# Optimization experiments

Hardware: AMD Instinct MI355X
Metric: run time of the kernel (lower is better)

Reference implementation:

```python
import jax, jax.numpy as jnp
import numpy as np

B, S, D = 4, 2048, 1024
H, HD = 16, 64  # heads, head_dim; H*HD == D


def setup_inputs() -> dict:
    key = jax.random.key(0)
    k_x, k_qkv, k_proj = jax.random.split(key, 3)
    x = jax.random.normal(k_x, (B, S, D), dtype=jnp.float32)
    # init scale ~ 1/sqrt(fan_in) to keep activations sane
    w_qkv = jax.random.normal(k_qkv, (D, 3 * H * HD), dtype=jnp.float32) / np.sqrt(D)
    b_qkv = jnp.zeros((3 * H * HD,), dtype=jnp.float32)
    w_proj = jax.random.normal(k_proj, (H * HD, D), dtype=jnp.float32) / np.sqrt(H * HD)
    b_proj = jnp.zeros((D,), dtype=jnp.float32)
    return {"x": x, "w_qkv": w_qkv, "b_qkv": b_qkv, "w_proj": w_proj,
            "b_proj": b_proj, "layer_idx": 0}


def reference(x, w_qkv, b_qkv, w_proj, b_proj, layer_idx):
    # c_attn: [B,S,D] -> [B,S,3*H*HD]
    qkv = x @ w_qkv + b_qkv
    qkv = qkv.reshape(B, S, 3, H, HD)
    q, k, v = qkv[:, :, 0], qkv[:, :, 1], qkv[:, :, 2]  # each [B,S,H,HD]

    scale = jax.lax.rsqrt(float(HD))  # scale_by_inverse_layer_idx=False
    # scores: [B,H,S_q,S_k]
    scores = jnp.einsum("bqhd,bkhd->bhqk", q, k) * scale
    causal = jnp.tril(jnp.ones((S, S), dtype=jnp.bool_))
    scores = jnp.where(causal, scores, -1e9)
    attn = jax.nn.softmax(scores, axis=-1)  # dropout is identity (inference)

    out = jnp.einsum("bhqk,bkhd->bqhd", attn, v).reshape(B, S, H * HD)
    return out @ w_proj + b_proj
```

## Files before the change

### kernel.cpp

```cpp
#include <hip/hip_runtime.h>

typedef __attribute__((ext_vector_type(8))) short short8;
typedef __attribute__((ext_vector_type(4))) float f32x4;
typedef __attribute__((ext_vector_type(16))) float f32x16;
typedef __attribute__((ext_vector_type(4))) float flt4;
typedef __attribute__((ext_vector_type(4))) unsigned int u32x4;
typedef unsigned short bfbits;

#define DEVI __device__ __forceinline__

constexpr int Bc = 4, Sc = 2048, Dc = 1024, Hc = 16, HDc = 64;
constexpr int M1 = Bc * Sc;
constexpr int N1 = 3 * Hc * HDc;
constexpr int Kd = Dc;

typedef __attribute__((address_space(1))) const unsigned int gas_u32;
typedef __attribute__((address_space(3))) unsigned int las_u32;

DEVI void gld_lds16(const void* g, void* l) {
  __builtin_amdgcn_global_load_lds((gas_u32*)g, (las_u32*)l, 16, 0, 0);
}

DEVI unsigned short f2bf(float f) {
  unsigned int x = __builtin_bit_cast(unsigned int, f);
  x = x + 0x7fffu + ((x >> 16) & 1u);
  return (unsigned short)(x >> 16);
}

DEVI f32x4 zero4() { f32x4 z = {0.f, 0.f, 0.f, 0.f}; return z; }

DEVI short8 lds8(const void* base, int byteoff) {
  return *(const short8*)((const char*)base + byteoff);
}

DEVI unsigned int cvtpk_bf16(float lo, float hi) {
  unsigned int r;
  asm("v_cvt_pk_bf16_f32 %0, %1, %2" : "=v"(r) : "v"(lo), "v"(hi));
  return r;
}

DEVI void pl32swap(unsigned int& dst, unsigned int& src) {
  asm volatile("v_permlane32_swap_b32 %0, %1" : "+v"(dst), "+v"(src));
}

__global__ void cast_x_kernel(const float* __restrict__ in, bfbits* __restrict__ out, int n8) {
  int i = blockIdx.x * 256 + threadIdx.x;
  if (i >= n8) return;
  const flt4* p = (const flt4*)in;
  flt4 a = p[(size_t)2 * i];
  flt4 b = p[(size_t)2 * i + 1];
  short8 r;
  r[0] = (short)f2bf(a[0]); r[1] = (short)f2bf(a[1]);
  r[2] = (short)f2bf(a[2]); r[3] = (short)f2bf(a[3]);
  r[4] = (short)f2bf(b[0]); r[5] = (short)f2bf(b[1]);
  r[6] = (short)f2bf(b[2]); r[7] = (short)f2bf(b[3]);
  *(short8*)(out + (size_t)8 * i) = r;
}

__global__ void transpose_cast_kernel(const float* __restrict__ in, bfbits* __restrict__ out,
                                      int R, int C) {
  __shared__ float tile[32][33];
  int bc = blockIdx.x * 32, br = blockIdx.y * 32;
  int tx = threadIdx.x & 31, ty = threadIdx.x >> 5;
#pragma unroll
  for (int i = 0; i < 32; i += 8)
    tile[ty + i][tx] = in[(size_t)(br + ty + i) * C + bc + tx];
  __syncthreads();
#pragma unroll
  for (int i = 0; i < 32; i += 8)
    out[(size_t)(bc + ty + i) * R + br + tx] = f2bf(tile[tx][ty + i]);
}

template <int EPI>
__global__ __launch_bounds__(256, 2) void gemm_bt_kernel(
    const bfbits* __restrict__ A, const bfbits* __restrict__ Bt,
    const float* __restrict__ bias,
    bfbits* __restrict__ outQ, bfbits* __restrict__ outK, bfbits* __restrict__ outV,
    float* __restrict__ outF, int M, int N, int K) {
  __shared__ bfbits sA[128 * 64];
  __shared__ bfbits sB[128 * 64];
  const int t = threadIdx.x;
  const int wid = t >> 6, l = t & 63;
  const int lr = l & 15, lg = l >> 4;
  const int m0 = blockIdx.y * 128, n0 = blockIdx.x * 128;
  const int wr = (wid >> 1) * 64, wc = (wid & 1) * 64;

  f32x4 acc[4][4];
#pragma unroll
  for (int i = 0; i < 4; ++i)
#pragma unroll
    for (int j = 0; j < 4; ++j) acc[i][j] = zero4();

  const int row_s = t >> 3;
  const int grp_s = t & 7;

  for (int kt = 0; kt < K; kt += 64) {
#pragma unroll
    for (int i = 0; i < 4; ++i) {
      int row = i * 32 + row_s;
      int grp = grp_s ^ (row & 7);
      gld_lds16(A + (size_t)(m0 + row) * K + kt + grp * 8, sA + i * 2048 + wid * 512);
      gld_lds16(Bt + (size_t)(n0 + row) * K + kt + grp * 8, sB + i * 2048 + wid * 512);
    }
    __syncthreads();
#pragma unroll
    for (int ks = 0; ks < 2; ++ks) {
      short8 af[4], bf[4];
#pragma unroll
      for (int i = 0; i < 4; ++i) {
        int rA = wr + i * 16 + lr;
        af[i] = lds8(sA, rA * 128 + (((ks * 4 + lg) ^ (rA & 7)) << 4));
        int rB = wc + i * 16 + lr;
        bf[i] = lds8(sB, rB * 128 + (((ks * 4 + lg) ^ (rB & 7)) << 4));
      }
#pragma unroll
      for (int i = 0; i < 4; ++i)
#pragma unroll
        for (int j = 0; j < 4; ++j)
          acc[i][j] = __builtin_amdgcn_mfma_f32_16x16x32_bf16(af[i], bf[j], acc[i][j], 0, 0, 0);
    }
    __syncthreads();
  }

#pragma unroll
  for (int i = 0; i < 4; ++i) {
#pragma unroll
    for (int j = 0; j < 4; ++j) {
#pragma unroll
      for (int r = 0; r < 4; ++r) {
        int row = m0 + wr + i * 16 + lg * 4 + r;
        int col = n0 + wc + j * 16 + lr;
        float v = acc[i][j][r] + bias[col];
        if (EPI == 0) {
          int which = col >> 10;
          int h = (col >> 6) & 15;
          int d = col & 63;
          int b = row >> 11;
          int s = row & 2047;
          bfbits bv = f2bf(v);
          if (which == 0) {
            outQ[((size_t)(b * 16 + h) * 2048 + s) * 64 + d] = bv;
          } else if (which == 1) {
            outK[((size_t)(b * 16 + h) * 2048 + s) * 64 + d] = bv;
          } else {
            outV[((size_t)(b * 16 + h) * 64 + d) * 2048 + s] = bv;
          }
        } else {
          outF[(size_t)row * N + col] = v;
        }
      }
    }
  }
}

__global__ __launch_bounds__(256, 2) void attn_kernel(
    const bfbits* __restrict__ Q, const bfbits* __restrict__ K,
    const bfbits* __restrict__ Vt, bfbits* __restrict__ O) {
  __shared__ bfbits sK[64 * 64];
  __shared__ bfbits sV[64 * 64];

  const int t = threadIdx.x, wid = t >> 6, l = t & 63;
  const int lq = l & 31, b5 = l >> 5;

  const int id = blockIdx.x;
  const int swz = (id & 7) * 64 + (id >> 3);
  const int pr = swz & 7;
  const int bh = swz >> 3;
  const int b = bh >> 4, h = bh & 15;

  const bfbits* Qb = Q + (size_t)bh * Sc * HDc;
  const bfbits* Kb = K + (size_t)bh * Sc * HDc;
  const bfbits* Vtb = Vt + (size_t)bh * Sc * HDc;

  const float cscale = 0.125f * 1.4426950408889634f;
  const int row_s = t >> 3, grp_s = t & 7;

  for (int half = 0; half < 2; ++half) {
    const int qt = half ? (15 - pr) : pr;
    const int qb = qt * 128;
    const int qrow = qb + wid * 32 + lq;
    const int qmaxw = qb + wid * 32 + 31;

    short8 qf[4];
#pragma unroll
    for (int ds = 0; ds < 4; ++ds)
      qf[ds] = *(const short8*)(Qb + (size_t)qrow * 64 + ds * 16 + b5 * 8);

    f32x16 acc0 = {0.f, 0.f, 0.f, 0.f, 0.f, 0.f, 0.f, 0.f,
                   0.f, 0.f, 0.f, 0.f, 0.f, 0.f, 0.f, 0.f};
    f32x16 acc1 = acc0;
    float mrow = 0.f, lrow = 0.f;

    const int nkv = 2 * (qt + 1);
    for (int kb = 0; kb < nkv; ++kb) {
      const int kv0 = kb * 64;
#pragma unroll
      for (int i = 0; i < 2; ++i) {
        int rr = i * 32 + row_s;
        int grp = grp_s ^ (rr & 7);
        gld_lds16(Kb + (size_t)(kv0 + rr) * 64 + grp * 8, sK + i * 2048 + wid * 512);
        gld_lds16(Vtb + (size_t)rr * Sc + kv0 + grp * 8, sV + i * 2048 + wid * 512);
      }
      __syncthreads();

      if (kv0 <= qmaxw) {
#pragma unroll
        for (int sub = 0; sub < 2; ++sub) {
          const int kvb = kv0 + sub * 32;
          if (kvb <= qmaxw) {
            f32x16 st = {0.f, 0.f, 0.f, 0.f, 0.f, 0.f, 0.f, 0.f,
                         0.f, 0.f, 0.f, 0.f, 0.f, 0.f, 0.f, 0.f};
            const int rK = sub * 32 + lq;
            const int swK = rK & 7;
#pragma unroll
            for (int ds = 0; ds < 4; ++ds) {
              short8 kf = lds8(sK, rK * 128 + (((ds * 2 + b5) ^ swK) << 4));
              st = __builtin_amdgcn_mfma_f32_32x32x16_bf16(kf, qf[ds], st, 0, 0, 0);
            }
            if (kvb + 31 > qb + wid * 32) {
#pragma unroll
              for (int r = 0; r < 16; ++r) {
                int kvi = kvb + (r & 3) + 8 * (r >> 2) + 4 * b5;
                st[r] = (kvi > qrow) ? -1e30f : st[r] * cscale;
              }
            } else {
#pragma unroll
              for (int r = 0; r < 16; ++r) st[r] *= cscale;
            }
            float mx = st[0];
#pragma unroll
            for (int r = 1; r < 16; ++r) mx = fmaxf(mx, st[r]);
            mx = fmaxf(mx, __shfl_xor(mx, 32));
            if (__any(mx > mrow + 8.f)) {
              float mnew = fmaxf(mrow, mx);
              float sold = exp2f(mrow - mnew);
              mrow = mnew;
              lrow *= sold;
#pragma unroll
              for (int r = 0; r < 16; ++r) {
                float sb = __shfl(sold, (r & 3) + 8 * (r >> 2) + 4 * b5, 32);
                acc0[r] *= sb;
                acc1[r] *= sb;
              }
            }
            float ssum = 0.f;
#pragma unroll
            for (int r = 0; r < 16; ++r) {
              float p = exp2f(st[r] - mrow);
              st[r] = p;
              ssum += p;
            }
            lrow += ssum;
            unsigned int W0 = cvtpk_bf16(st[0], st[1]);
            unsigned int W1 = cvtpk_bf16(st[2], st[3]);
            unsigned int W2 = cvtpk_bf16(st[4], st[5]);
            unsigned int W3 = cvtpk_bf16(st[6], st[7]);
            unsigned int W4 = cvtpk_bf16(st[8], st[9]);
            unsigned int W5 = cvtpk_bf16(st[10], st[11]);
            unsigned int W6 = cvtpk_bf16(st[12], st[13]);
            unsigned int W7 = cvtpk_bf16(st[14], st[15]);
            pl32swap(W0, W2);
            pl32swap(W1, W3);
            pl32swap(W4, W6);
            pl32swap(W5, W7);
            u32x4 pa0u = {W0, W1, W2, W3};
            u32x4 pa1u = {W4, W5, W6, W7};
            short8 pa0 = __builtin_bit_cast(short8, pa0u);
            short8 pa1 = __builtin_bit_cast(short8, pa1u);
#pragma unroll
            for (int dt = 0; dt < 2; ++dt) {
              int rv = dt * 32 + lq;
              int swV = rv & 7;
              short8 vf0 = lds8(sV, rv * 128 + (((sub * 4 + 0 + b5) ^ swV) << 4));
              short8 vf1 = lds8(sV, rv * 128 + (((sub * 4 + 2 + b5) ^ swV) << 4));
              if (dt == 0) {
                acc0 = __builtin_amdgcn_mfma_f32_32x32x16_bf16(pa0, vf0, acc0, 0, 0, 0);
                acc0 = __builtin_amdgcn_mfma_f32_32x32x16_bf16(pa1, vf1, acc0, 0, 0, 0);
              } else {
                acc1 = __builtin_amdgcn_mfma_f32_32x32x16_bf16(pa0, vf0, acc1, 0, 0, 0);
                acc1 = __builtin_amdgcn_mfma_f32_32x32x16_bf16(pa1, vf1, acc1, 0, 0, 0);
              }
            }
          }
        }
      }
      __syncthreads();
    }

    float lsum = lrow + __shfl_xor(lrow, 32);
    float inv = 1.0f / lsum;
#pragma unroll
    for (int r = 0; r < 16; ++r) {
      int qrel = (r & 3) + 8 * (r >> 2) + 4 * b5;
      float ib = __shfl(inv, qrel, 32);
      int srow = qb + wid * 32 + qrel;
      size_t base = (size_t)(b * Sc + srow) * (Hc * HDc) + h * 64;
      O[base + lq] = f2bf(acc0[r] * ib);
      O[base + 32 + lq] = f2bf(acc1[r] * ib);
    }
  }
}

extern "C" void kernel_launch(void* const* d_in, const int* in_sizes, int n_in,
                              void* d_out, int out_size, void* d_ws, size_t ws_size,
                              hipStream_t stream) {
  const float* x = (const float*)d_in[0];
  const float* w_qkv = (const float*)d_in[1];
  const float* b_qkv = (const float*)d_in[2];
  const float* w_proj = (const float*)d_in[3];
  const float* b_proj = (const float*)d_in[4];
  float* out = (float*)d_out;

  char* ws = (char*)d_ws;
  size_t off = 0;
  auto alloc = [&](size_t bytes) {
    char* p = ws + off;
    off = off + ((bytes + 255) & ~(size_t)255);
    return p;
  };
  bfbits* Xb = (bfbits*)alloc((size_t)M1 * Kd * 2);
  bfbits* WqkvT = (bfbits*)alloc((size_t)N1 * Kd * 2);
  bfbits* WprojT = (bfbits*)alloc((size_t)Dc * Dc * 2);
  bfbits* Qb = (bfbits*)alloc((size_t)Bc * Hc * Sc * HDc * 2);
  bfbits* Kb = (bfbits*)alloc((size_t)Bc * Hc * Sc * HDc * 2);
  bfbits* Vtb = (bfbits*)alloc((size_t)Bc * Hc * Sc * HDc * 2);
  bfbits* Ob = Xb;

  cast_x_kernel<<<(M1 * Kd / 8 + 255) / 256, 256, 0, stream>>>(x, Xb, M1 * Kd / 8);
  transpose_cast_kernel<<<dim3(N1 / 32, Kd / 32), 256, 0, stream>>>(w_qkv, WqkvT, Kd, N1);
  transpose_cast_kernel<<<dim3(Dc / 32, Dc / 32), 256, 0, stream>>>(w_proj, WprojT, Dc, Dc);

  gemm_bt_kernel<0><<<dim3(N1 / 128, M1 / 128), 256, 0, stream>>>(
      Xb, WqkvT, b_qkv, Qb, Kb, Vtb, nullptr, M1, N1, Kd);

  attn_kernel<<<dim3(512), 256, 0, stream>>>(Qb, Kb, Vtb, Ob);

  gemm_bt_kernel<1><<<dim3(Dc / 128, M1 / 128), 256, 0, stream>>>(
      Ob, WprojT, b_proj, nullptr, nullptr, nullptr, out, M1, Dc, Kd);
}
```

Baseline: 271.7 us.

## Double-buffer K/V tiles in attention, fold softmax scale into Q

The attention loop now uses two LDS buffers for K and V and issues the async global-to-LDS load of the next tile before computing on the current one, so the load overlaps with compute and one barrier per iteration is removed. The softmax scale (1/sqrt(d) times log2 e) is applied to Q in the QKV GEMM epilogue rather than to every score tile. s_setprio is raised around the MFMA blocks. LDS use doubles, which could limit occupancy, and rounding Q to bf16 after scaling slightly changes numerics.

```diff
diff --git a/kernel.cpp b/kernel.cpp
--- a/kernel.cpp
+++ b/kernel.cpp
@@ -13,6 +13,7 @@
 constexpr int M1 = Bc * Sc;
 constexpr int N1 = 3 * Hc * HDc;
 constexpr int Kd = Dc;
+constexpr float QSCALE = 0.125f * 1.4426950408889634f;
 
 typedef __attribute__((address_space(1))) const unsigned int gas_u32;
 typedef __attribute__((address_space(3))) unsigned int las_u32;
@@ -137,13 +138,12 @@
           int d = col & 63;
           int b = row >> 11;
           int s = row & 2047;
-          bfbits bv = f2bf(v);
           if (which == 0) {
-            outQ[((size_t)(b * 16 + h) * 2048 + s) * 64 + d] = bv;
+            outQ[((size_t)(b * 16 + h) * 2048 + s) * 64 + d] = f2bf(v * QSCALE);
           } else if (which == 1) {
-            outK[((size_t)(b * 16 + h) * 2048 + s) * 64 + d] = bv;
+            outK[((size_t)(b * 16 + h) * 2048 + s) * 64 + d] = f2bf(v);
           } else {
-            outV[((size_t)(b * 16 + h) * 64 + d) * 2048 + s] = bv;
+            outV[((size_t)(b * 16 + h) * 64 + d) * 2048 + s] = f2bf(v);
           }
         } else {
           outF[(size_t)row * N + col] = v;
@@ -156,8 +156,8 @@
 __global__ __launch_bounds__(256, 2) void attn_kernel(
     const bfbits* __restrict__ Q, const bfbits* __restrict__ K,
     const bfbits* __restrict__ Vt, bfbits* __restrict__ O) {
-  __shared__ bfbits sK[64 * 64];
-  __shared__ bfbits sV[64 * 64];
+  __shared__ bfbits sK[2 * 64 * 64];
+  __shared__ bfbits sV[2 * 64 * 64];
 
   const int t = threadIdx.x, wid = t >> 6, l = t & 63;
   const int lq = l & 31, b5 = l >> 5;
@@ -172,8 +172,20 @@
   const bfbits* Kb = K + (size_t)bh * Sc * HDc;
   const bfbits* Vtb = Vt + (size_t)bh * Sc * HDc;
 
-  const float cscale = 0.125f * 1.4426950408889634f;
   const int row_s = t >> 3, grp_s = t & 7;
+
+  auto STAGE = [&](int kb, int bufi) {
+    const int kv0s = kb * 64;
+#pragma unroll
+    for (int i = 0; i < 2; ++i) {
+      int rr = i * 32 + row_s;
+      int grp = grp_s ^ (rr & 7);
+      gld_lds16(Kb + (size_t)(kv0s + rr) * 64 + grp * 8,
+                sK + bufi * 4096 + i * 2048 + wid * 512);
+      gld_lds16(Vtb + (size_t)rr * Sc + kv0s + grp * 8,
+                sV + bufi * 4096 + i * 2048 + wid * 512);
+    }
+  };
 
   for (int half = 0; half < 2; ++half) {
     const int qt = half ? (15 - pr) : pr;
@@ -192,16 +204,15 @@
     float mrow = 0.f, lrow = 0.f;
 
     const int nkv = 2 * (qt + 1);
+    int cur = 0;
+    STAGE(0, 0);
+    __syncthreads();
+
     for (int kb = 0; kb < nkv; ++kb) {
       const int kv0 = kb * 64;
-#pragma unroll
-      for (int i = 0; i < 2; ++i) {
-        int rr = i * 32 + row_s;
-        int grp = grp_s ^ (rr & 7);
-        gld_lds16(Kb + (size_t)(kv0 + rr) * 64 + grp * 8, sK + i * 2048 + wid * 512);
-        gld_lds16(Vtb + (size_t)rr * Sc + kv0 + grp * 8, sV + i * 2048 + wid * 512);
-      }
-      __syncthreads();
+      if (kb + 1 < nkv) STAGE(kb + 1, cur ^ 1);
+      const bfbits* bK = sK + cur * 4096;
+      const bfbits* bV = sV + cur * 4096;
 
       if (kv0 <= qmaxw) {
 #pragma unroll
@@ -212,20 +223,19 @@
                          0.f, 0.f, 0.f, 0.f, 0.f, 0.f, 0.f, 0.f};
             const int rK = sub * 32 + lq;
             const int swK = rK & 7;
+            __builtin_amdgcn_s_setprio(1);
 #pragma unroll
             for (int ds = 0; ds < 4; ++ds) {
-              short8 kf = lds8(sK, rK * 128 + (((ds * 2 + b5) ^ swK) << 4));
+              short8 kf = lds8(bK, rK * 128 + (((ds * 2 + b5) ^ swK) << 4));
               st = __builtin_amdgcn_mfma_f32_32x32x16_bf16(kf, qf[ds], st, 0, 0, 0);
             }
+            __builtin_amdgcn_s_setprio(0);
             if (kvb + 31 > qb + wid * 32) {
 #pragma unroll
               for (int r = 0; r < 16; ++r) {
                 int kvi = kvb + (r & 3) + 8 * (r >> 2) + 4 * b5;
-                st[r] = (kvi > qrow) ? -1e30f : st[r] * cscale;
+                st[r] = (kvi > qrow) ? -1e30f : st[r];
               }
-            } else {
-#pragma unroll
-              for (int r = 0; r < 16; ++r) st[r] *= cscale;
             }
             float mx = st[0];
 #pragma unroll
@@ -267,12 +277,13 @@
             u32x4 pa1u = {W4, W5, W6, W7};
             short8 pa0 = __builtin_bit_cast(short8, pa0u);
             short8 pa1 = __builtin_bit_cast(short8, pa1u);
+            __builtin_amdgcn_s_setprio(1);
 #pragma unroll
             for (int dt = 0; dt < 2; ++dt) {
               int rv = dt * 32 + lq;
               int swV = rv & 7;
-              short8 vf0 = lds8(sV, rv * 128 + (((sub * 4 + 0 + b5) ^ swV) << 4));
-              short8 vf1 = lds8(sV, rv * 128 + (((sub * 4 + 2 + b5) ^ swV) << 4));
+              short8 vf0 = lds8(bV, rv * 128 + (((sub * 4 + 0 + b5) ^ swV) << 4));
+              short8 vf1 = lds8(bV, rv * 128 + (((sub * 4 + 2 + b5) ^ swV) << 4));
               if (dt == 0) {
                 acc0 = __builtin_amdgcn_mfma_f32_32x32x16_bf16(pa0, vf0, acc0, 0, 0, 0);
                 acc0 = __builtin_amdgcn_mfma_f32_32x32x16_bf16(pa1, vf1, acc0, 0, 0, 0);
@@ -281,10 +292,12 @@
                 acc1 = __builtin_amdgcn_mfma_f32_32x32x16_bf16(pa1, vf1, acc1, 0, 0, 0);
               }
             }
+            __builtin_amdgcn_s_setprio(0);
           }
         }
       }
       __syncthreads();
+      cur ^= 1;
     }
 
     float lsum = lrow + __shfl_xor(lrow, 32);
```

New measurement: 275.9 us. Within noise of the previous version (+1.5%).
